# Kernel tuning notes

Hardware: AMD Instinct MI355X
Metric: run time of the kernel (lower is better)

The kernel has to match this reference:

```python
import jax, jax.numpy as jnp
import numpy as np
from jax import lax

G, DIM, E, K, OC = 8, 32, 8, 2, 10  # groups, per-group channels, experts, top-k, out_channels


def setup_inputs() -> dict:
    key = jax.random.key(0)
    ks = jax.random.split(key, 6)
    B, L = 64, 4096
    x = jax.random.normal(ks[0], (B, G * DIM, L), dtype=jnp.float32)
    conv1_w = jax.random.normal(ks[1], (G * OC, DIM, 3), dtype=jnp.float32) * 0.05
    conv1_b = jax.random.normal(ks[2], (G * OC,), dtype=jnp.float32) * 0.05
    conv2_w = jax.random.normal(ks[3], (G * OC * E, OC, 1), dtype=jnp.float32) * 0.1
    conv2_b = jax.random.normal(ks[4], (G * OC * E,), dtype=jnp.float32) * 0.05
    w_gate = jax.random.normal(ks[5], (G, DIM * 5, E), dtype=jnp.float32) * 0.05
    return {"x": x, "conv1_w": conv1_w, "conv1_b": conv1_b,
            "conv2_w": conv2_w, "conv2_b": conv2_b, "w_gate": w_gate}


def _cv_squared(v):
    # torch .var() is unbiased (ddof=1)
    return jnp.var(v, ddof=1) / (jnp.mean(v) ** 2 + 1e-10)


def reference(x, conv1_w, conv1_b, conv2_w, conv2_b, w_gate):
    B, C, L = x.shape
    loss_coef = 0.01

    # ---- noisy_top_k_gating (eval path: no noise) per group, vectorized ----
    # gating input: last-6..last-1 timesteps of each group -> [B, G, DIM*5]
    gin = x.reshape(B, G, DIM, L)[:, :, :, -6:-1].reshape(B, G, DIM * 5)
    clean_logits = jnp.einsum('bgd,gde->bge', gin, w_gate)      # [B,G,E]
    probs = jax.nn.softmax(clean_logits, axis=-1)
    top_vals, top_idx = lax.top_k(probs, K)                      # [B,G,K]
    top_gates = top_vals / (jnp.sum(top_vals, axis=-1, keepdims=True) + 1e-6)
    onehot = jax.nn.one_hot(top_idx, E, dtype=probs.dtype)       # [B,G,K,E]
    gates = jnp.einsum('bgke,bgk->bge', onehot, top_gates)       # [B,G,E]

    load = jnp.sum(gates > 0, axis=0).astype(jnp.float32)        # [G,E]
    importance = jnp.sum(gates, axis=0)                          # [G,E]
    out_loss = loss_coef * (jax.vmap(_cv_squared)(importance).sum()
                            + jax.vmap(_cv_squared)(load).sum())

    # ---- per-group expert conv stacks as grouped conv1d ----
    dn = ('NCH', 'OIH', 'NCH')
    h = lax.conv_general_dilated(x, conv1_w, (1,), 'VALID',
                                 dimension_numbers=dn, feature_group_count=G)
    h = jnp.tanh(h + conv1_b[None, :, None])                     # [B, G*OC, L-2]
    o = lax.conv_general_dilated(h, conv2_w, (1,), 'VALID',
                                 dimension_numbers=dn, feature_group_count=G)
    o = o + conv2_b[None, :, None]                               # [B, G*OC*E, L']
    Lp = o.shape[-1]
    o = o.reshape(B, G, OC, E, Lp)  # channel c within group = d*E + e (matches torch reshape)

    # einsum 'BLDE,BE->BLD' then permute -> [B, G, OC, L']
    combine_features = jnp.einsum('bgdel,bge->bgdl', o, gates)
    gates_out = jnp.transpose(gates, (0, 2, 1))                  # [B, E, G]
    return combine_features, out_loss, gates_out
```

## Files before the change

kernel.cpp:

```cpp
#include <hip/hip_runtime.h>
#include <cmath>

#define B_    64
#define G_    8
#define E_    8
#define OC_   10
#define LL    4096
#define LP    4094
#define COMBINE_SIZE (B_ * G_ * OC_ * LP)
#define SLOT  4096

typedef float f32x2 __attribute__((ext_vector_type(2)));

__device__ __forceinline__ float fast_tanh(float v) {
    const float e = __expf(2.f * v);
    return 1.f - 2.f * __builtin_amdgcn_rcpf(e + 1.f);
}

__device__ __forceinline__ int gswz(int g) {
    const int c = g & 63;
    return (g & ~63) | (c ^ (c >> 3));
}

__global__ void repack_kernel(const float* __restrict__ w1,
                              float* __restrict__ w1t) {
    const int i = blockIdx.x * 256 + threadIdx.x;
    if (i >= G_ * 32 * 30) return;
    const int g = i / 960, r = i - g * 960;
    const int d = r / 30,  s = r - d * 30;
    const int o = s / 3,   t = s - o * 3;
    w1t[g * 1024 + d * 32 + s] = w1[g * 960 + o * 96 + d * 3 + t];
}

__global__ void loss_kernel(const float* __restrict__ gws,
                            float* __restrict__ loss_out) {
    const int tid = threadIdx.x;
    float imp = 0.f, ld = 0.f;
    for (int b = 0; b < B_; ++b) {
        const float v = gws[b * 64 + tid];
        imp += v;
        ld  += (v > 0.f) ? 1.f : 0.f;
    }
    float si = imp, sl = ld;
    #pragma unroll
    for (int msk = 1; msk <= 4; msk <<= 1) { si += __shfl_xor(si, msk); sl += __shfl_xor(sl, msk); }
    const float mi = si * 0.125f, ml = sl * 0.125f;
    float di = imp - mi, dl = ld - ml;
    float vi = di * di, vl = dl * dl;
    #pragma unroll
    for (int msk = 1; msk <= 4; msk <<= 1) { vi += __shfl_xor(vi, msk); vl += __shfl_xor(vl, msk); }
    const float cvi = (vi / 7.f) / (mi * mi + 1e-10f);
    const float cvl = (vl / 7.f) / (ml * ml + 1e-10f);
    float c = ((tid & 7) == 0) ? (cvi + cvl) : 0.f;
    #pragma unroll
    for (int msk = 1; msk < 64; msk <<= 1) c += __shfl_xor(c, msk);
    if (tid == 0) *loss_out = 0.01f * c;
}

__global__ __launch_bounds__(512, 4) void conv_kernel(
        const float* __restrict__ x,
        const float* __restrict__ w1t,
        const float* __restrict__ b1,
        const float* __restrict__ w2, const float* __restrict__ b2,
        const float* __restrict__ wg,
        float* __restrict__ out,
        float* __restrict__ gws,
        float* __restrict__ gout) {
    const int tid  = threadIdx.x;
    const int lane = tid & 63;
    const int wq   = tid >> 6;
    const int bg   = blockIdx.x;
    const int g    = bg & 7;
    const int b    = bg >> 3;

    __shared__ float  ring[4][SLOT];
    __shared__ float2 halo[8][32];
    __shared__ float  gin[160];
    __shared__ float  gg[E_];
    __shared__ float  weff[OC_ * OC_];
    __shared__ float  beff[OC_];

    const float* xrow = x + (size_t)bg * 32 * LL;

    if (tid < 160) {
        const int d = tid / 5, t = tid - 5 * d;
        gin[tid] = xrow[(size_t)d * LL + (LL - 6 + t)];
    }
    __syncthreads();

    if (tid < 64) {
        const int e = tid & 7, part = tid >> 3;
        const float* wp = wg + g * 1280 + e;
        float logit = 0.f;
        #pragma unroll
        for (int i = 0; i < 20; ++i) {
            const int idx = part * 20 + i;
            logit = fmaf(gin[idx], wp[idx * 8], logit);
        }
        logit += __shfl_xor(logit, 8);
        logit += __shfl_xor(logit, 16);
        logit += __shfl_xor(logit, 32);
        float m = logit;
        #pragma unroll
        for (int s = 4; s >= 1; s >>= 1) m = fmaxf(m, __shfl_xor(m, s));
        float p = expf(logit - m);
        float sum = p;
        #pragma unroll
        for (int s = 4; s >= 1; s >>= 1) sum += __shfl_xor(sum, s);
        p /= sum;
        if (tid < 8) {
            float pv[8];
            #pragma unroll
            for (int j = 0; j < 8; ++j) pv[j] = __shfl(p, j);
            int i1 = 0; float v1 = pv[0];
            #pragma unroll
            for (int j = 1; j < 8; ++j) if (pv[j] > v1) { v1 = pv[j]; i1 = j; }
            int i2 = -1; float v2 = -1.f;
            #pragma unroll
            for (int j = 0; j < 8; ++j) if (j != i1 && pv[j] > v2) { v2 = pv[j]; i2 = j; }
            const float denom = v1 + v2 + 1e-6f;
            const float gate = (e == i1) ? v1 / denom
                             : ((e == i2) ? v2 / denom : 0.f);
            gg[e] = gate;
            gws[bg * E_ + e] = gate;
            gout[b * 64 + e * 8 + g] = gate;
        }
    }
    if (lane < 32) {
        const float* hp = xrow + (size_t)lane * LL + (wq < 7 ? wq * 512 + 512 : 0);
        halo[wq][lane] = *reinterpret_cast<const float2*>(hp);
    }
    __syncthreads();

    if (tid < 100) {
        const int dd = tid / 10, j = tid - dd * 10;
        float s = 0.f;
        #pragma unroll
        for (int e = 0; e < 8; ++e)
            s = fmaf(gg[e], w2[(g * 80 + dd * 8 + e) * 10 + j], s);
        weff[tid] = s;
    } else if (tid < 110) {
        const int dd = tid - 100;
        float s = 0.f;
        #pragma unroll
        for (int e = 0; e < 8; ++e)
            s = fmaf(gg[e], b2[g * 80 + dd * 8 + e], s);
        beff[dd] = s;
    }

    const float* wgt = w1t + g * 1024;
    const float* b1g = b1 + g * OC_;

    const int sl = (lane ^ (lane >> 3)) * 4;

#define STAGE(r)                                                              \
    {                                                                         \
        const float* gb = xrow + (size_t)(r) * LL + wq * 512;                 \
        float* lb = &ring[(r) & 3][wq * 512];                                 \
        __builtin_amdgcn_global_load_lds(                                     \
            (const __attribute__((address_space(1))) void*)(gb + sl),         \
            (__attribute__((address_space(3))) void*)lb, 16, 0, 0);           \
        __builtin_amdgcn_global_load_lds(                                     \
            (const __attribute__((address_space(1))) void*)(gb + 256 + sl),   \
            (__attribute__((address_space(3))) void*)(lb + 256), 16, 0, 0);   \
    }

#define WAITV(n) asm volatile("s_waitcnt vmcnt(" #n ")" ::: "memory");

    f32x2 acc2[10][4];
    #pragma unroll
    for (int o = 0; o < 10; ++o) {
        const float bv = b1g[o];
        #pragma unroll
        for (int q = 0; q < 4; ++q) acc2[o][q] = (f32x2){bv, bv};
    }

    const int p1 = gswz(tid * 2) * 4;
    const int p2 = gswz(tid * 2 + 1) * 4;
    const bool l63 = (lane == 63);

#define COMPROW(dd)                                                           \
    {                                                                         \
        const float* sb = ring[(dd) & 3];                                     \
        float xw[10];                                                         \
        *reinterpret_cast<float4*>(&xw[0]) =                                  \
            *reinterpret_cast<const float4*>(sb + p1);                        \
        *reinterpret_cast<float4*>(&xw[4]) =                                  \
            *reinterpret_cast<const float4*>(sb + p2);                        \
        const float2 hv = halo[wq][(dd)];                                     \
        const float n0 = __shfl_down(xw[0], 1);                               \
        const float n1 = __shfl_down(xw[1], 1);                               \
        xw[8] = l63 ? hv.x : n0;                                              \
        xw[9] = l63 ? hv.y : n1;                                              \
        f32x2 xv[5], xb[4];                                                   \
        _Pragma("unroll")                                                     \
        for (int q = 0; q < 5; ++q) xv[q] = (f32x2){xw[2*q], xw[2*q+1]};      \
        _Pragma("unroll")                                                     \
        for (int q = 0; q < 4; ++q) xb[q] = (f32x2){xw[2*q+1], xw[2*q+2]};    \
        const float* wr = wgt + (dd) * 32;                                    \
        _Pragma("unroll")                                                     \
        for (int o = 0; o < 10; ++o) {                                        \
            const float w0 = wr[o * 3];                                       \
            const float wA = wr[o * 3 + 1];                                   \
            const float wB = wr[o * 3 + 2];                                   \
            const f32x2 W0 = {w0, w0}, WA = {wA, wA}, WB = {wB, wB};          \
            _Pragma("unroll")                                                 \
            for (int q = 0; q < 4; ++q)                                       \
                acc2[o][q] = __builtin_elementwise_fma(xv[q + 1], WB,         \
                             __builtin_elementwise_fma(xb[q],     WA,         \
                             __builtin_elementwise_fma(xv[q],     W0,         \
                                                       acc2[o][q])));         \
        }                                                                     \
    }

    STAGE(0) STAGE(1) STAGE(2)

    #pragma unroll 1
    for (int d = 0; d < 29; ++d) {
        WAITV(4)
        COMPROW(d)
        STAGE(d + 3)
    }
    WAITV(4) COMPROW(29)
    WAITV(2) COMPROW(30)
    WAITV(0) COMPROW(31)

#undef STAGE
#undef WAITV
#undef COMPROW

    #pragma unroll
    for (int o = 0; o < 10; ++o)
        #pragma unroll
        for (int q = 0; q < 4; ++q) {
            acc2[o][q][0] = fast_tanh(acc2[o][q][0]);
            acc2[o][q][1] = fast_tanh(acc2[o][q][1]);
        }

    __syncthreads();

    const int l = tid * 8;
    float* ob = out + (size_t)bg * OC_ * LP + l;
    const bool full = (l + 8 <= LP);
    #pragma unroll
    for (int dd = 0; dd < 10; ++dd) {
        const float* wr = weff + dd * 10;
        const float bv = beff[dd];
        f32x2 r2[4];
        #pragma unroll
        for (int q = 0; q < 4; ++q) r2[q] = (f32x2){bv, bv};
        #pragma unroll
        for (int j = 0; j < 10; ++j) {
            const float w = wr[j];
            const f32x2 W = {w, w};
            #pragma unroll
            for (int q = 0; q < 4; ++q)
                r2[q] = __builtin_elementwise_fma(acc2[j][q], W, r2[q]);
        }
        float* op = ob + (size_t)dd * LP;
        if (full) {
            #pragma unroll
            for (int q = 0; q < 4; ++q)
                *reinterpret_cast<float2*>(op + 2 * q) =
                    make_float2(r2[q][0], r2[q][1]);
        } else {
            #pragma unroll
            for (int q = 0; q < 4; ++q) {
                if (l + 2 * q     < LP) op[2 * q]     = r2[q][0];
                if (l + 2 * q + 1 < LP) op[2 * q + 1] = r2[q][1];
            }
        }
    }
}

extern "C" void kernel_launch(void* const* d_in, const int* in_sizes, int n_in,
                              void* d_out, int out_size, void* d_ws, size_t ws_size,
                              hipStream_t stream) {
    (void)in_sizes; (void)n_in; (void)out_size; (void)ws_size;
    const float* x  = (const float*)d_in[0];
    const float* w1 = (const float*)d_in[1];
    const float* b1 = (const float*)d_in[2];
    const float* w2 = (const float*)d_in[3];
    const float* b2 = (const float*)d_in[4];
    const float* wg = (const float*)d_in[5];
    float* out      = (float*)d_out;
    float* gws      = (float*)d_ws;
    float* w1t      = (float*)d_ws + B_ * G_ * E_;
    float* loss_out = out + COMBINE_SIZE;
    float* gout     = out + COMBINE_SIZE + 1;

    repack_kernel<<<(G_ * 32 * 30 + 255) / 256, 256, 0, stream>>>(w1, w1t);
    conv_kernel<<<B_ * G_, 512, 0, stream>>>(x, w1t, b1, w2, b2, wg,
                                             out, gws, gout);
    loss_kernel<<<1, 64, 0, stream>>>(gws, loss_out);
}
```

Before: 100.0 us.

## Issue gating, halo and first stages as async LDS loads up front; defer weff

Moves the gating-input and halo reads to direct global-to-LDS async loads and issues the first three ring stages before the gating computation, so the prologue latency overlaps with the streaming pipeline. The synchronization is reduced to a vmcnt wait plus a raw s_barrier. The weff/beff mixing is moved after the conv loop, so it no longer sits on the critical path before the main stream. This relies on tight vmcnt accounting and on the LDS layout written by the 4-byte global_load_lds, and getting either wrong would risk correctness.

```diff
diff --git a/kernel.cpp b/kernel.cpp
--- a/kernel.cpp
+++ b/kernel.cpp
@@ -11,6 +11,8 @@
 #define SLOT  4096
 
 typedef float f32x2 __attribute__((ext_vector_type(2)));
+#define AS1 __attribute__((address_space(1)))
+#define AS3 __attribute__((address_space(3)))
 
 __device__ __forceinline__ float fast_tanh(float v) {
     const float e = __expf(2.f * v);
@@ -75,18 +77,46 @@
 
     __shared__ float  ring[4][SLOT];
     __shared__ float2 halo[8][32];
-    __shared__ float  gin[160];
+    __shared__ float  gin[192];
     __shared__ float  gg[E_];
     __shared__ float  weff[OC_ * OC_];
     __shared__ float  beff[OC_];
 
     const float* xrow = x + (size_t)bg * 32 * LL;
+    const int sl = (lane ^ (lane >> 3)) * 4;
+
+#define STAGE(r)                                                              \
+    {                                                                         \
+        const float* gb = xrow + (size_t)(r) * LL + wq * 512;                 \
+        float* lb = &ring[(r) & 3][wq * 512];                                 \
+        __builtin_amdgcn_global_load_lds(                                     \
+            (const AS1 void*)(gb + sl),                                       \
+            (AS3 void*)lb, 16, 0, 0);                                         \
+        __builtin_amdgcn_global_load_lds(                                     \
+            (const AS1 void*)(gb + 256 + sl),                                 \
+            (AS3 void*)(lb + 256), 16, 0, 0);                                 \
+    }
+
+#define WAITV(n) asm volatile("s_waitcnt vmcnt(" #n ")" ::: "memory");
 
     if (tid < 160) {
-        const int d = tid / 5, t = tid - 5 * d;
-        gin[tid] = xrow[(size_t)d * LL + (LL - 6 + t)];
-    }
-    __syncthreads();
+        const int dd = tid / 5, t = tid - 5 * dd;
+        __builtin_amdgcn_global_load_lds(
+            (const AS1 void*)(xrow + (size_t)dd * LL + (LL - 6 + t)),
+            (AS3 void*)(gin + (wq << 6)), 4, 0, 0);
+    }
+    {
+        const int hr = lane >> 1, hc = lane & 1;
+        const float* hsrc = xrow + (size_t)hr * LL
+                          + (wq < 7 ? wq * 512 + 512 + hc : hc);
+        __builtin_amdgcn_global_load_lds(
+            (const AS1 void*)hsrc,
+            (AS3 void*)(reinterpret_cast<float*>(halo) + (wq << 6)), 4, 0, 0);
+    }
+    STAGE(0) STAGE(1) STAGE(2)
+
+    WAITV(6)
+    __builtin_amdgcn_s_barrier();
 
     if (tid < 64) {
         const int e = tid & 7, part = tid >> 3;
@@ -126,46 +156,11 @@
             gout[b * 64 + e * 8 + g] = gate;
         }
     }
-    if (lane < 32) {
-        const float* hp = xrow + (size_t)lane * LL + (wq < 7 ? wq * 512 + 512 : 0);
-        halo[wq][lane] = *reinterpret_cast<const float2*>(hp);
-    }
-    __syncthreads();
-
-    if (tid < 100) {
-        const int dd = tid / 10, j = tid - dd * 10;
-        float s = 0.f;
-        #pragma unroll
-        for (int e = 0; e < 8; ++e)
-            s = fmaf(gg[e], w2[(g * 80 + dd * 8 + e) * 10 + j], s);
-        weff[tid] = s;
-    } else if (tid < 110) {
-        const int dd = tid - 100;
-        float s = 0.f;
-        #pragma unroll
-        for (int e = 0; e < 8; ++e)
-            s = fmaf(gg[e], b2[g * 80 + dd * 8 + e], s);
-        beff[dd] = s;
-    }
-
+    asm volatile("s_waitcnt lgkmcnt(0)" ::: "memory");
+    __builtin_amdgcn_s_barrier();
+
+    const float* b1g = b1 + g * OC_;
     const float* wgt = w1t + g * 1024;
-    const float* b1g = b1 + g * OC_;
-
-    const int sl = (lane ^ (lane >> 3)) * 4;
-
-#define STAGE(r)                                                              \
-    {                                                                         \
-        const float* gb = xrow + (size_t)(r) * LL + wq * 512;                 \
-        float* lb = &ring[(r) & 3][wq * 512];                                 \
-        __builtin_amdgcn_global_load_lds(                                     \
-            (const __attribute__((address_space(1))) void*)(gb + sl),         \
-            (__attribute__((address_space(3))) void*)lb, 16, 0, 0);           \
-        __builtin_amdgcn_global_load_lds(                                     \
-            (const __attribute__((address_space(1))) void*)(gb + 256 + sl),   \
-            (__attribute__((address_space(3))) void*)(lb + 256), 16, 0, 0);   \
-    }
-
-#define WAITV(n) asm volatile("s_waitcnt vmcnt(" #n ")" ::: "memory");
 
     f32x2 acc2[10][4];
     #pragma unroll
@@ -213,8 +208,6 @@
         }                                                                     \
     }
 
-    STAGE(0) STAGE(1) STAGE(2)
-
     #pragma unroll 1
     for (int d = 0; d < 29; ++d) {
         WAITV(4)
@@ -237,6 +230,21 @@
             acc2[o][q][1] = fast_tanh(acc2[o][q][1]);
         }
 
+    if (tid < 100) {
+        const int dd = tid / 10, j = tid - dd * 10;
+        float s = 0.f;
+        #pragma unroll
+        for (int e = 0; e < 8; ++e)
+            s = fmaf(gg[e], w2[(g * 80 + dd * 8 + e) * 10 + j], s);
+        weff[tid] = s;
+    } else if (tid < 110) {
+        const int dd = tid - 100;
+        float s = 0.f;
+        #pragma unroll
+        for (int e = 0; e < 8; ++e)
+            s = fmaf(gg[e], b2[g * 80 + dd * 8 + e], s);
+        beff[dd] = s;
+    }
     __syncthreads();
 
     const int l = tid * 8;
```

Result: no change. 98.98 us (-1.1%).
